# Performance work log

Measured on AMD Instinct MI355X. Metric: run time of the kernel, lower is better.

The kernel has to match this reference:

```python
import jax, jax.numpy as jnp
import numpy as np

B, S, E, H, L = 16, 1024, 512, 8, 4
D = E // H  # head_dim = 64


def setup_inputs() -> dict:
    key = jax.random.key(0)
    ks = jax.random.split(key, 16)
    std = 0.02
    inp = {
        "q": jax.random.normal(ks[0], (B, S, E), jnp.float32),
        "k": jax.random.normal(ks[1], (B, S, E), jnp.float32),
        "v": jax.random.normal(ks[2], (B, S, E), jnp.float32),
        # standard Linear params (torch convention: W is (out, in))
        "Wq": jax.random.normal(ks[3], (E, E), jnp.float32) * std,
        "bq": jnp.zeros((E,), jnp.float32),
        "Wk": jax.random.normal(ks[4], (E, E), jnp.float32) * std,
        "bk": jnp.zeros((E,), jnp.float32),
        # WFLinear: shared weight elementwise-multiplied by per-language factor
        "Wv_share": jax.random.normal(ks[5], (E, E), jnp.float32) * std,
        "Wv_spec": 1.0 + jax.random.normal(ks[6], (L, E, E), jnp.float32) * std,
        "bv_share": jnp.zeros((E,), jnp.float32),
        "bv_spec": jax.random.normal(ks[7], (L, E), jnp.float32) * std,
        "Wo_share": jax.random.normal(ks[8], (E, E), jnp.float32) * std,
        "Wo_spec": 1.0 + jax.random.normal(ks[9], (L, E, E), jnp.float32) * std,
        "bo_share": jnp.zeros((E,), jnp.float32),
        "bo_spec": jax.random.normal(ks[10], (L, E), jnp.float32) * std,
        "mask": jax.random.randint(ks[11], (B, S), 0, 2, jnp.int32),
        "languageID": 1,
    }
    return inp


def reference(q, k, v, Wq, bq, Wk, bk, Wv_share, Wv_spec, bv_share, bv_spec,
              Wo_share, Wo_spec, bo_share, bo_spec, mask, languageID):
    scaling = D ** (-0.5)
    # projections (torch Linear: x @ W.T + b)
    Q = (q @ Wq.T + bq).reshape(B, S, H, D).transpose(0, 2, 1, 3) * scaling
    K = (k @ Wk.T + bk).reshape(B, S, H, D).transpose(0, 2, 1, 3)
    Wv = Wv_share * Wv_spec[languageID]
    bv = bv_share + bv_spec[languageID]
    V = (v @ Wv.T + bv).reshape(B, S, H, D).transpose(0, 2, 1, 3)
    # NOTE: faithful to original — Q already scaled by d_k^-0.5, and
    # AttentionWF divides by sqrt(d_k) AGAIN (effective scale 1/d_k).
    alpha = jnp.einsum("bhqd,bhkd->bhqk", Q, K) / np.float32(np.sqrt(D))
    m = (mask == 0)[:, None, None, :]  # (B,1,1,S) over key axis
    alpha = jnp.where(m, jnp.float32(-1e9), alpha)
    alpha = jax.nn.softmax(alpha, axis=-1)
    # dropout p=0.0 -> identity
    ctx = jnp.einsum("bhqk,bhkd->bhqd", alpha, V)  # (B,H,S,D)
    concat = ctx.transpose(0, 2, 1, 3).reshape(B, S, E)
    Wo = Wo_share * Wo_spec[languageID]
    bo = bo_share + bo_spec[languageID]
    return concat @ Wo.T + bo
```

## Files before the change

kernel.cpp:

```cpp
#include <hip/hip_runtime.h>

#define B_ 16
#define S_ 1024
#define E_ 512
#define H_ 8
#define D_ 64
#define L_ 4
#define M_ (B_*S_)

typedef unsigned short u16;
typedef __attribute__((ext_vector_type(8))) short bf16x8;
typedef __attribute__((ext_vector_type(4))) float f32x4;
typedef __attribute__((ext_vector_type(4))) unsigned uint4v;

__device__ __forceinline__ u16 f2bf(float x) {
  unsigned u = __float_as_uint(x);
  unsigned r = (u + 0x7fffu + ((u >> 16) & 1u)) >> 16;
  return (u16)r;
}
__device__ __forceinline__ ushort4 f2bf4(float4 f) {
  ushort4 u;
  u.x = f2bf(f.x); u.y = f2bf(f.y); u.z = f2bf(f.z); u.w = f2bf(f.w);
  return u;
}
__device__ __forceinline__ unsigned pk_bf16(float lo, float hi) {
  unsigned ul = __float_as_uint(lo) + 0x8000u;
  unsigned uh = __float_as_uint(hi) + 0x8000u;
#if __has_builtin(__builtin_amdgcn_perm)
  return __builtin_amdgcn_perm(uh, ul, 0x07060302u);
#else
  return (ul >> 16) | (uh & 0xffff0000u);
#endif
}

typedef __attribute__((address_space(1))) const void gconst_void;
typedef __attribute__((address_space(3))) void lds_void;
__device__ __forceinline__ void gl_lds16(const void* g, void* l) {
  __builtin_amdgcn_global_load_lds((gconst_void*)g, (lds_void*)l, 16, 0, 0);
}

__global__ __launch_bounds__(256) void prep_w(
    const float* __restrict__ Wq, const float* __restrict__ Wk,
    const float* __restrict__ Wv_sh, const float* __restrict__ Wv_sp,
    const float* __restrict__ Wo_sh, const float* __restrict__ Wo_sp,
    const float* __restrict__ bv_sh, const float* __restrict__ bv_sp,
    const float* __restrict__ bo_sh, const float* __restrict__ bo_sp,
    const int* __restrict__ langp,
    u16* __restrict__ Wq_b, u16* __restrict__ Wk_b,
    u16* __restrict__ Wv_b, u16* __restrict__ Wo_b,
    float* __restrict__ bv_f, float* __restrict__ bo_f) {
  int lang = langp[0];
  int i = blockIdx.x * 256 + threadIdx.x;
  size_t wofs = (size_t)lang * (E_*E_/4) + i;
  ((ushort4*)Wq_b)[i] = f2bf4(((const float4*)Wq)[i]);
  ((ushort4*)Wk_b)[i] = f2bf4(((const float4*)Wk)[i]);
  float4 vs = ((const float4*)Wv_sh)[i], vp = ((const float4*)Wv_sp)[wofs];
  float4 os = ((const float4*)Wo_sh)[i], op = ((const float4*)Wo_sp)[wofs];
  float4 vv = {vs.x*vp.x, vs.y*vp.y, vs.z*vp.z, vs.w*vp.w};
  float4 oo = {os.x*op.x, os.y*op.y, os.z*op.z, os.w*op.w};
  ((ushort4*)Wv_b)[i] = f2bf4(vv);
  ((ushort4*)Wo_b)[i] = f2bf4(oo);
  if (i < E_/4) {
    float4 b1 = ((const float4*)bv_sh)[i], b2 = ((const float4*)(bv_sp + (size_t)lang*E_))[i];
    float4 b3 = ((const float4*)bo_sh)[i], b4 = ((const float4*)(bo_sp + (size_t)lang*E_))[i];
    float4 r1 = {b1.x+b2.x, b1.y+b2.y, b1.z+b2.z, b1.w+b2.w};
    float4 r2 = {b3.x+b4.x, b3.y+b4.y, b3.z+b4.z, b3.w+b4.w};
    ((float4*)bv_f)[i] = r1;
    ((float4*)bo_f)[i] = r2;
  }
}

__global__ __launch_bounds__(256) void gemm_qkv(
    const float* __restrict__ q, const float* __restrict__ k, const float* __restrict__ v,
    const u16* __restrict__ Wq_b, const u16* __restrict__ Wk_b, const u16* __restrict__ Wv_b,
    const float* __restrict__ bq, const float* __restrict__ bk, const float* __restrict__ bv,
    u16* __restrict__ Qb, u16* __restrict__ Kb, u16* __restrict__ Vb) {
  __shared__ __align__(16) float sAf[128*32];
  __shared__ __align__(16) u16 sB[128*32];
  const int z = blockIdx.z;
  const float* A    = (z == 0) ? q : (z == 1) ? k : v;
  const u16*   Bw   = (z == 0) ? Wq_b : (z == 1) ? Wk_b : Wv_b;
  const float* bias = (z == 0) ? bq : (z == 1) ? bk : bv;
  u16*         out  = (z == 0) ? Qb : (z == 1) ? Kb : Vb;
  const int t = threadIdx.x;
  const int m0 = blockIdx.y * 128, n0 = blockIdx.x * 128;
  const int lane = t & 63, wid = t >> 6;
  const int m16 = lane & 15, qq = lane >> 4;
  const int wrow = (wid >> 1) * 64, wcol = (wid & 1) * 64;
  f32x4 acc[4][4] = {};
  const int ca0 = wid*4;
  const float* ap[4];
  float* sap[4];
#pragma unroll
  for (int i = 0; i < 4; ++i) {
    int ca = ca0 + i;
    ap[i]  = A + (size_t)(m0 + ca*8 + (lane >> 3)) * E_ + (lane & 7) * 4;
    sap[i] = &sAf[ca * 256];
  }
  const int cb0 = wid*2, cb1 = wid*2 + 1;
  const u16* bp0 = Bw + (size_t)(n0 + cb0*16 + (lane >> 2)) * E_ + (lane & 3) * 8;
  const u16* bp1 = Bw + (size_t)(n0 + cb1*16 + (lane >> 2)) * E_ + (lane & 3) * 8;
  u16* sbp0 = &sB[cb0 * 512];
  u16* sbp1 = &sB[cb1 * 512];
  for (int k0 = 0; k0 < E_; k0 += 32) {
#pragma unroll
    for (int i = 0; i < 4; ++i) gl_lds16(ap[i], sap[i]);
    gl_lds16(bp0, sbp0);
    gl_lds16(bp1, sbp1);
    __syncthreads();
    bf16x8 af[4], bfm[4];
#pragma unroll
    for (int mt = 0; mt < 4; ++mt) {
      const float* ar = &sAf[(wrow + mt*16 + m16) * 32 + qq*8];
      f32x4 a0 = *(const f32x4*)ar;
      f32x4 a1 = *(const f32x4*)(ar + 4);
      union { uint4v u; bf16x8 h; } cv;
      cv.u = (uint4v){ pk_bf16(a0[0], a0[1]), pk_bf16(a0[2], a0[3]),
                       pk_bf16(a1[0], a1[1]), pk_bf16(a1[2], a1[3]) };
      af[mt] = cv.h;
    }
#pragma unroll
    for (int nt = 0; nt < 4; ++nt)
      bfm[nt] = *(const bf16x8*)&sB[(wcol + nt*16 + m16) * 32 + qq*8];
#pragma unroll
    for (int mt = 0; mt < 4; ++mt)
#pragma unroll
      for (int nt = 0; nt < 4; ++nt)
        acc[mt][nt] = __builtin_amdgcn_mfma_f32_16x16x32_bf16(af[mt], bfm[nt], acc[mt][nt], 0, 0, 0);
    __syncthreads();
#pragma unroll
    for (int i = 0; i < 4; ++i) ap[i] += 32;
    bp0 += 32; bp1 += 32;
  }
  float bvv[4];
#pragma unroll
  for (int nt = 0; nt < 4; ++nt) bvv[nt] = bias[n0 + wcol + nt*16 + m16];
#pragma unroll
  for (int mt = 0; mt < 4; ++mt) {
    int gm = m0 + wrow + mt*16 + qq*4;
#pragma unroll
    for (int nt = 0; nt < 4; ++nt) {
      int gn = n0 + wcol + nt*16 + m16;
#pragma unroll
      for (int r = 0; r < 4; ++r)
        out[(size_t)(gm + r) * E_ + gn] = f2bf(acc[mt][nt][r] + bvv[nt]);
    }
  }
}

__global__ __launch_bounds__(256) void gemm_lds(
    const u16* __restrict__ A, const u16* __restrict__ Bw,
    const float* __restrict__ bias, float* __restrict__ out) {
  __shared__ __align__(16) u16 sA[128*32];
  __shared__ __align__(16) u16 sB[128*32];
  const int t = threadIdx.x;
  const int m0 = blockIdx.y * 128, n0 = blockIdx.x * 128;
  const int lane = t & 63, wid = t >> 6;
  const int m16 = lane & 15, qq = lane >> 4;
  const int wrow = (wid >> 1) * 64, wcol = (wid & 1) * 64;
  f32x4 acc[4][4] = {};
  const int c0 = 2*wid, c1 = 2*wid + 1;
  const int colk = (lane & 3) * 8;
  const int r0 = c0*16 + (lane >> 2), r1 = c1*16 + (lane >> 2);
  const u16* a0 = A  + (size_t)(m0 + r0) * E_ + colk;
  const u16* a1 = A  + (size_t)(m0 + r1) * E_ + colk;
  const u16* b0 = Bw + (size_t)(n0 + r0) * E_ + colk;
  const u16* b1 = Bw + (size_t)(n0 + r1) * E_ + colk;
  u16* sa0 = &sA[c0*512]; u16* sa1 = &sA[c1*512];
  u16* sb0 = &sB[c0*512]; u16* sb1 = &sB[c1*512];
  for (int k0 = 0; k0 < E_; k0 += 32) {
    gl_lds16(a0, sa0);
    gl_lds16(a1, sa1);
    gl_lds16(b0, sb0);
    gl_lds16(b1, sb1);
    __syncthreads();
    bf16x8 af[4], bfm[4];
#pragma unroll
    for (int mt = 0; mt < 4; ++mt)
      af[mt] = *(const bf16x8*)&sA[(wrow + mt*16 + m16) * 32 + qq*8];
#pragma unroll
    for (int nt = 0; nt < 4; ++nt)
      bfm[nt] = *(const bf16x8*)&sB[(wcol + nt*16 + m16) * 32 + qq*8];
#pragma unroll
    for (int mt = 0; mt < 4; ++mt)
#pragma unroll
      for (int nt = 0; nt < 4; ++nt)
        acc[mt][nt] = __builtin_amdgcn_mfma_f32_16x16x32_bf16(af[mt], bfm[nt], acc[mt][nt], 0, 0, 0);
    __syncthreads();
    a0 += 32; a1 += 32; b0 += 32; b1 += 32;
  }
  float bv[4];
#pragma unroll
  for (int nt = 0; nt < 4; ++nt) bv[nt] = bias[n0 + wcol + nt*16 + m16];
#pragma unroll
  for (int mt = 0; mt < 4; ++mt) {
    int gm = m0 + wrow + mt*16 + qq*4;
#pragma unroll
    for (int nt = 0; nt < 4; ++nt) {
      int gn = n0 + wcol + nt*16 + m16;
#pragma unroll
      for (int r = 0; r < 4; ++r)
        out[(size_t)(gm + r) * E_ + gn] = acc[mt][nt][r] + bv[nt];
    }
  }
}

#define TS_ 72
__global__ __launch_bounds__(256) void transpose_v(const u16* __restrict__ Vb,
                                                   u16* __restrict__ Vt) {
  __shared__ __align__(16) u16 sT[64*TS_];
  const int t = threadIdx.x;
  const int bh = blockIdx.y, b = bh >> 3, h = bh & 7;
  const int s0 = blockIdx.x * 64;
  const int row = t >> 2, c0 = (t & 3) * 16;
  const u16* src = Vb + (size_t)(b*S_ + s0 + row) * E_ + h*D_ + c0;
  *(uint4*)&sT[row*TS_ + c0]     = *(const uint4*)src;
  *(uint4*)&sT[row*TS_ + c0 + 8] = *(const uint4*)(src + 8);
  __syncthreads();
  const int d = t >> 2, sc = (t & 3) * 16;
  unsigned w[8];
#pragma unroll
  for (int i = 0; i < 8; ++i) {
    unsigned lo = sT[(sc + 2*i    ) * TS_ + d];
    unsigned hi = sT[(sc + 2*i + 1) * TS_ + d];
    w[i] = lo | (hi << 16);
  }
  u16* dst = Vt + ((size_t)(b*H_ + h) * D_ + d) * S_ + s0 + sc;
  uint4 p0 = {w[0], w[1], w[2], w[3]}, p1 = {w[4], w[5], w[6], w[7]};
  *(uint4*)dst = p0;
  *(uint4*)(dst + 8) = p1;
}

#define KST 72
__global__ __launch_bounds__(256) void attn_mfma(
    const u16* __restrict__ Qb, const u16* __restrict__ Kb, const u16* __restrict__ Vt,
    const int* __restrict__ mask, u16* __restrict__ ctxb) {
  __shared__ __align__(16) u16 sK[64*KST];
  __shared__ __align__(16) u16 sV[64*KST];
  __shared__ __align__(16) u16 sP[64*KST];
  __shared__ __align__(16) float sMask[64];
  __shared__ __align__(16) float sL[64];
  const int t = threadIdx.x;
  const int lane = t & 63, w = t >> 6;
  const int m16 = lane & 15, quad = lane >> 4;
  const int bh = blockIdx.y, b = bh >> 3, h = bh & 7;
  const int qblk = blockIdx.x * 64;
  const int q0 = qblk + w * 16;
  bf16x8 qf0, qf1;
  {
    const u16* qp = Qb + (size_t)(b*S_ + q0 + m16) * E_ + h*D_ + quad*8;
    qf0 = *(const bf16x8*)qp;
    qf1 = *(const bf16x8*)(qp + 32);
  }
  f32x4 oacc[4] = {};
  float lpart = 0.f;
  const int srow = t >> 2, sc0 = (t & 3) * 16;
  const u16* kp = Kb + (size_t)(b*S_ + srow) * E_ + h*D_ + sc0;
  const u16* vp = Vt + ((size_t)(b*H_ + h) * D_ + srow) * S_ + sc0;
  uint4 rk0 = *(const uint4*)kp, rk1 = *(const uint4*)(kp + 8);
  uint4 rv0 = *(const uint4*)vp, rv1 = *(const uint4*)(vp + 8);
  float rmsk = 0.f;
  if (t < 64) rmsk = (mask[b*S_ + t] == 0) ? -1e9f : 0.f;
  const float CS = 0.015625f * 1.44269504f;
  for (int kt = 0; kt < S_; kt += 64) {
    *(uint4*)&sK[srow*KST + sc0]     = rk0;
    *(uint4*)&sK[srow*KST + sc0 + 8] = rk1;
    *(uint4*)&sV[srow*KST + sc0]     = rv0;
    *(uint4*)&sV[srow*KST + sc0 + 8] = rv1;
    if (t < 64) sMask[t] = rmsk;
    __syncthreads();
    if (kt + 64 < S_) {
      kp += (size_t)64 * E_; vp += 64;
      rk0 = *(const uint4*)kp; rk1 = *(const uint4*)(kp + 8);
      rv0 = *(const uint4*)vp; rv1 = *(const uint4*)(vp + 8);
      if (t < 64) rmsk = (mask[b*S_ + kt + 64 + t] == 0) ? -1e9f : 0.f;
    }
    f32x4 sacc[4] = {};
#pragma unroll
    for (int ct = 0; ct < 4; ++ct) {
      bf16x8 kf0 = *(const bf16x8*)&sK[(ct*16 + m16)*KST + quad*8];
      bf16x8 kf1 = *(const bf16x8*)&sK[(ct*16 + m16)*KST + 32 + quad*8];
      sacc[ct] = __builtin_amdgcn_mfma_f32_16x16x32_bf16(kf0, qf0, sacc[ct], 0, 0, 0);
      sacc[ct] = __builtin_amdgcn_mfma_f32_16x16x32_bf16(kf1, qf1, sacc[ct], 0, 0, 0);
    }
#pragma unroll
    for (int ct = 0; ct < 4; ++ct) {
      f32x4 msk = *(const f32x4*)&sMask[ct*16 + quad*4];
      float p0 = exp2f(fmaf(sacc[ct][0], CS, msk[0]));
      float p1 = exp2f(fmaf(sacc[ct][1], CS, msk[1]));
      float p2 = exp2f(fmaf(sacc[ct][2], CS, msk[2]));
      float p3 = exp2f(fmaf(sacc[ct][3], CS, msk[3]));
      lpart += (p0 + p1) + (p2 + p3);
      uint2 pq = { pk_bf16(p0, p1), pk_bf16(p2, p3) };
      *(uint2*)&sP[(w*16 + m16)*KST + ct*16 + quad*4] = pq;
    }
    bf16x8 pf0 = *(const bf16x8*)&sP[(w*16 + m16)*KST + quad*8];
    bf16x8 pf1 = *(const bf16x8*)&sP[(w*16 + m16)*KST + 32 + quad*8];
#pragma unroll
    for (int dt = 0; dt < 4; ++dt) {
      bf16x8 vf0 = *(const bf16x8*)&sV[(dt*16 + m16)*KST + quad*8];
      bf16x8 vf1 = *(const bf16x8*)&sV[(dt*16 + m16)*KST + 32 + quad*8];
      oacc[dt] = __builtin_amdgcn_mfma_f32_16x16x32_bf16(pf0, vf0, oacc[dt], 0, 0, 0);
      oacc[dt] = __builtin_amdgcn_mfma_f32_16x16x32_bf16(pf1, vf1, oacc[dt], 0, 0, 0);
    }
    __syncthreads();
  }
  lpart += __shfl_xor(lpart, 16);
  lpart += __shfl_xor(lpart, 32);
  if (quad == 0) sL[w*16 + m16] = lpart;
  float inv[4];
#pragma unroll
  for (int r = 0; r < 4; ++r) inv[r] = 1.0f / sL[w*16 + quad*4 + r];
#pragma unroll
  for (int dt = 0; dt < 4; ++dt)
#pragma unroll
    for (int r = 0; r < 4; ++r)
      sP[(w*16 + quad*4 + r)*KST + dt*16 + m16] = f2bf(oacc[dt][r] * inv[r]);
  __syncthreads();
  const int orow = t >> 2, oc0 = (t & 3) * 16;
  uint4 o0 = *(uint4*)&sP[orow*KST + oc0];
  uint4 o1 = *(uint4*)&sP[orow*KST + oc0 + 8];
  u16* dst = ctxb + (size_t)(b*S_ + qblk + orow) * E_ + h*D_ + oc0;
  *(uint4*)dst = o0;
  *(uint4*)(dst + 8) = o1;
}

extern "C" void kernel_launch(void* const* d_in, const int* in_sizes, int n_in,
                              void* d_out, int out_size, void* d_ws, size_t ws_size,
                              hipStream_t stream) {
  const float* q     = (const float*)d_in[0];
  const float* k     = (const float*)d_in[1];
  const float* v     = (const float*)d_in[2];
  const float* Wq    = (const float*)d_in[3];
  const float* bq    = (const float*)d_in[4];
  const float* Wk    = (const float*)d_in[5];
  const float* bk    = (const float*)d_in[6];
  const float* Wv_sh = (const float*)d_in[7];
  const float* Wv_sp = (const float*)d_in[8];
  const float* bv_sh = (const float*)d_in[9];
  const float* bv_sp = (const float*)d_in[10];
  const float* Wo_sh = (const float*)d_in[11];
  const float* Wo_sp = (const float*)d_in[12];
  const float* bo_sh = (const float*)d_in[13];
  const float* bo_sp = (const float*)d_in[14];
  const int*   mask  = (const int*)d_in[15];
  const int*   lang  = (const int*)d_in[16];

  char* ws = (char*)d_ws;
  size_t off = 0;
  auto alloc = [&](size_t bytes) -> char* {
    char* p = ws + off;
    off += (bytes + 255) & ~(size_t)255;
    return p;
  };
  u16* Qb   = (u16*)alloc((size_t)M_ * E_ * 2);
  u16* Kb   = (u16*)alloc((size_t)M_ * E_ * 2);
  u16* Vb   = (u16*)alloc((size_t)M_ * E_ * 2);
  u16* Vt   = (u16*)alloc((size_t)M_ * E_ * 2);
  u16* ctxb = (u16*)alloc((size_t)M_ * E_ * 2);
  u16* Wq_b = (u16*)alloc((size_t)E_ * E_ * 2);
  u16* Wk_b = (u16*)alloc((size_t)E_ * E_ * 2);
  u16* Wv_b = (u16*)alloc((size_t)E_ * E_ * 2);
  u16* Wo_b = (u16*)alloc((size_t)E_ * E_ * 2);
  float* bv_f = (float*)alloc(E_ * 4);
  float* bo_f = (float*)alloc(E_ * 4);

  prep_w<<<E_*E_/1024, 256, 0, stream>>>(Wq, Wk, Wv_sh, Wv_sp, Wo_sh, Wo_sp,
                                         bv_sh, bv_sp, bo_sh, bo_sp, lang,
                                         Wq_b, Wk_b, Wv_b, Wo_b, bv_f, bo_f);

  dim3 qkvgrid(E_/128, M_/128, 3);
  gemm_qkv<<<qkvgrid, 256, 0, stream>>>(q, k, v, Wq_b, Wk_b, Wv_b,
                                        bq, bk, bv_f, Qb, Kb, Vb);

  dim3 tgrid(S_/64, B_*H_);
  transpose_v<<<tgrid, 256, 0, stream>>>(Vb, Vt);

  dim3 agrid(S_/64, B_*H_);
  attn_mfma<<<agrid, 256, 0, stream>>>(Qb, Kb, Vt, mask, ctxb);

  dim3 ggrid(E_/128, M_/128);
  gemm_lds<<<ggrid, 256, 0, stream>>>(ctxb, Wo_b, bo_f, (float*)d_out);
}
```

Measured before the change: 316.9 us.

## Fuse V transpose into QKV GEMM, double K-step GEMMs, widen attention query tile

```diff
diff --git a/kernel.cpp b/kernel.cpp
--- a/kernel.cpp
+++ b/kernel.cpp
@@ -74,76 +74,110 @@
     const float* __restrict__ q, const float* __restrict__ k, const float* __restrict__ v,
     const u16* __restrict__ Wq_b, const u16* __restrict__ Wk_b, const u16* __restrict__ Wv_b,
     const float* __restrict__ bq, const float* __restrict__ bk, const float* __restrict__ bv,
-    u16* __restrict__ Qb, u16* __restrict__ Kb, u16* __restrict__ Vb) {
-  __shared__ __align__(16) float sAf[128*32];
-  __shared__ __align__(16) u16 sB[128*32];
+    u16* __restrict__ Qb, u16* __restrict__ Kb, u16* __restrict__ Vt) {
+  __shared__ __align__(16) float sAf[2*128*32];
+  __shared__ __align__(16) u16 sB[2*128*32];
   const int z = blockIdx.z;
   const float* A    = (z == 0) ? q : (z == 1) ? k : v;
   const u16*   Bw   = (z == 0) ? Wq_b : (z == 1) ? Wk_b : Wv_b;
   const float* bias = (z == 0) ? bq : (z == 1) ? bk : bv;
-  u16*         out  = (z == 0) ? Qb : (z == 1) ? Kb : Vb;
   const int t = threadIdx.x;
   const int m0 = blockIdx.y * 128, n0 = blockIdx.x * 128;
   const int lane = t & 63, wid = t >> 6;
   const int m16 = lane & 15, qq = lane >> 4;
   const int wrow = (wid >> 1) * 64, wcol = (wid & 1) * 64;
   f32x4 acc[4][4] = {};
-  const int ca0 = wid*4;
-  const float* ap[4];
-  float* sap[4];
-#pragma unroll
-  for (int i = 0; i < 4; ++i) {
-    int ca = ca0 + i;
-    ap[i]  = A + (size_t)(m0 + ca*8 + (lane >> 3)) * E_ + (lane & 7) * 4;
-    sap[i] = &sAf[ca * 256];
-  }
-  const int cb0 = wid*2, cb1 = wid*2 + 1;
-  const u16* bp0 = Bw + (size_t)(n0 + cb0*16 + (lane >> 2)) * E_ + (lane & 3) * 8;
-  const u16* bp1 = Bw + (size_t)(n0 + cb1*16 + (lane >> 2)) * E_ + (lane & 3) * 8;
-  u16* sbp0 = &sB[cb0 * 512];
-  u16* sbp1 = &sB[cb1 * 512];
-  for (int k0 = 0; k0 < E_; k0 += 32) {
-#pragma unroll
-    for (int i = 0; i < 4; ++i) gl_lds16(ap[i], sap[i]);
-    gl_lds16(bp0, sbp0);
-    gl_lds16(bp1, sbp1);
-    __syncthreads();
-    bf16x8 af[4], bfm[4];
+  const float* apg[2][4];
+  float* apl[2][4];
+#pragma unroll
+  for (int p = 0; p < 2; ++p)
+#pragma unroll
+    for (int i = 0; i < 4; ++i) {
+      int ca = wid*4 + i;
+      apg[p][i] = A + (size_t)(m0 + ca*8 + (lane >> 3)) * E_ + p*32 + (lane & 7) * 4;
+      apl[p][i] = &sAf[p*4096 + ca*256 + lane*4];
+    }
+  const u16* bpg[2][2];
+  u16* bpl[2][2];
+#pragma unroll
+  for (int p = 0; p < 2; ++p)
+#pragma unroll
+    for (int i = 0; i < 2; ++i) {
+      int cb = wid*2 + i;
+      bpg[p][i] = Bw + (size_t)(n0 + cb*16 + (lane >> 2)) * E_ + p*32 + (lane & 3) * 8;
+      bpl[p][i] = &sB[p*4096 + cb*512 + lane*8];
+    }
+  for (int k0 = 0; k0 < E_; k0 += 64) {
+#pragma unroll
+    for (int p = 0; p < 2; ++p) {
+#pragma unroll
+      for (int i = 0; i < 4; ++i) gl_lds16(apg[p][i], apl[p][i]);
+#pragma unroll
+      for (int i = 0; i < 2; ++i) gl_lds16(bpg[p][i], bpl[p][i]);
+    }
+    __syncthreads();
+#pragma unroll
+    for (int p = 0; p < 2; ++p) {
+      bf16x8 af[4], bfm[4];
+#pragma unroll
+      for (int mt = 0; mt < 4; ++mt) {
+        const float* ar = &sAf[p*4096 + (wrow + mt*16 + m16) * 32 + qq*8];
+        f32x4 a0 = *(const f32x4*)ar;
+        f32x4 a1 = *(const f32x4*)(ar + 4);
+        union { uint4v u; bf16x8 h; } cv;
+        cv.u = (uint4v){ pk_bf16(a0[0], a0[1]), pk_bf16(a0[2], a0[3]),
+                         pk_bf16(a1[0], a1[1]), pk_bf16(a1[2], a1[3]) };
+        af[mt] = cv.h;
+      }
+#pragma unroll
+      for (int nt = 0; nt < 4; ++nt)
+        bfm[nt] = *(const bf16x8*)&sB[p*4096 + (wcol + nt*16 + m16) * 32 + qq*8];
+#pragma unroll
+      for (int mt = 0; mt < 4; ++mt)
+#pragma unroll
+        for (int nt = 0; nt < 4; ++nt)
+          acc[mt][nt] = __builtin_amdgcn_mfma_f32_16x16x32_bf16(af[mt], bfm[nt], acc[mt][nt], 0, 0, 0);
+    }
+    __syncthreads();
+#pragma unroll
+    for (int p = 0; p < 2; ++p) {
+#pragma unroll
+      for (int i = 0; i < 4; ++i) apg[p][i] += 64;
+#pragma unroll
+      for (int i = 0; i < 2; ++i) bpg[p][i] += 64;
+    }
+  }
+  float bvv[4];
+#pragma unroll
+  for (int nt = 0; nt < 4; ++nt) bvv[nt] = bias[n0 + wcol + nt*16 + m16];
+  if (z < 2) {
+    u16* out = (z == 0) ? Qb : Kb;
 #pragma unroll
     for (int mt = 0; mt < 4; ++mt) {
-      const float* ar = &sAf[(wrow + mt*16 + m16) * 32 + qq*8];
-      f32x4 a0 = *(const f32x4*)ar;
-      f32x4 a1 = *(const f32x4*)(ar + 4);
-      union { uint4v u; bf16x8 h; } cv;
-      cv.u = (uint4v){ pk_bf16(a0[0], a0[1]), pk_bf16(a0[2], a0[3]),
-                       pk_bf16(a1[0], a1[1]), pk_bf16(a1[2], a1[3]) };
-      af[mt] = cv.h;
-    }
-#pragma unroll
-    for (int nt = 0; nt < 4; ++nt)
-      bfm[nt] = *(const bf16x8*)&sB[(wcol + nt*16 + m16) * 32 + qq*8];
-#pragma unroll
-    for (int mt = 0; mt < 4; ++mt)
-#pragma unroll
-      for (int nt = 0; nt < 4; ++nt)
-        acc[mt][nt] = __builtin_amdgcn_mfma_f32_16x16x32_bf16(af[mt], bfm[nt], acc[mt][nt], 0, 0, 0);
-    __syncthreads();
-#pragma unroll
-    for (int i = 0; i < 4; ++i) ap[i] += 32;
-    bp0 += 32; bp1 += 32;
-  }
-  float bvv[4];
-#pragma unroll
-  for (int nt = 0; nt < 4; ++nt) bvv[nt] = bias[n0 + wcol + nt*16 + m16];
-#pragma unroll
-  for (int mt = 0; mt < 4; ++mt) {
-    int gm = m0 + wrow + mt*16 + qq*4;
-#pragma unroll
-    for (int nt = 0; nt < 4; ++nt) {
-      int gn = n0 + wcol + nt*16 + m16;
-#pragma unroll
-      for (int r = 0; r < 4; ++r)
-        out[(size_t)(gm + r) * E_ + gn] = f2bf(acc[mt][nt][r] + bvv[nt]);
+      int gm = m0 + wrow + mt*16 + qq*4;
+#pragma unroll
+      for (int nt = 0; nt < 4; ++nt) {
+        int gn = n0 + wcol + nt*16 + m16;
+#pragma unroll
+        for (int r = 0; r < 4; ++r)
+          out[(size_t)(gm + r) * E_ + gn] = f2bf(acc[mt][nt][r] + bvv[nt]);
+      }
+    }
+  } else {
+#pragma unroll
+    for (int mt = 0; mt < 4; ++mt) {
+      int gm = m0 + wrow + mt*16 + qq*4;
+      int b = gm >> 10, s0 = gm & (S_ - 1);
+#pragma unroll
+      for (int nt = 0; nt < 4; ++nt) {
+        int gn = n0 + wcol + nt*16 + m16;
+        ushort4 u;
+        u.x = f2bf(acc[mt][nt][0] + bvv[nt]);
+        u.y = f2bf(acc[mt][nt][1] + bvv[nt]);
+        u.z = f2bf(acc[mt][nt][2] + bvv[nt]);
+        u.w = f2bf(acc[mt][nt][3] + bvv[nt]);
+        *(ushort4*)&Vt[((size_t)(b*E_ + gn)) * S_ + s0] = u;
+      }
     }
   }
 }
@@ -151,43 +185,55 @@
 __global__ __launch_bounds__(256) void gemm_lds(
     const u16* __restrict__ A, const u16* __restrict__ Bw,
     const float* __restrict__ bias, float* __restrict__ out) {
-  __shared__ __align__(16) u16 sA[128*32];
-  __shared__ __align__(16) u16 sB[128*32];
+  __shared__ __align__(16) u16 sA[2*128*32];
+  __shared__ __align__(16) u16 sB[2*128*32];
   const int t = threadIdx.x;
   const int m0 = blockIdx.y * 128, n0 = blockIdx.x * 128;
   const int lane = t & 63, wid = t >> 6;
   const int m16 = lane & 15, qq = lane >> 4;
   const int wrow = (wid >> 1) * 64, wcol = (wid & 1) * 64;
   f32x4 acc[4][4] = {};
-  const int c0 = 2*wid, c1 = 2*wid + 1;
-  const int colk = (lane & 3) * 8;
-  const int r0 = c0*16 + (lane >> 2), r1 = c1*16 + (lane >> 2);
-  const u16* a0 = A  + (size_t)(m0 + r0) * E_ + colk;
-  const u16* a1 = A  + (size_t)(m0 + r1) * E_ + colk;
-  const u16* b0 = Bw + (size_t)(n0 + r0) * E_ + colk;
-  const u16* b1 = Bw + (size_t)(n0 + r1) * E_ + colk;
-  u16* sa0 = &sA[c0*512]; u16* sa1 = &sA[c1*512];
-  u16* sb0 = &sB[c0*512]; u16* sb1 = &sB[c1*512];
-  for (int k0 = 0; k0 < E_; k0 += 32) {
-    gl_lds16(a0, sa0);
-    gl_lds16(a1, sa1);
-    gl_lds16(b0, sb0);
-    gl_lds16(b1, sb1);
-    __syncthreads();
-    bf16x8 af[4], bfm[4];
-#pragma unroll
-    for (int mt = 0; mt < 4; ++mt)
-      af[mt] = *(const bf16x8*)&sA[(wrow + mt*16 + m16) * 32 + qq*8];
-#pragma unroll
-    for (int nt = 0; nt < 4; ++nt)
-      bfm[nt] = *(const bf16x8*)&sB[(wcol + nt*16 + m16) * 32 + qq*8];
-#pragma unroll
-    for (int mt = 0; mt < 4; ++mt)
+  const u16* apg[2][2]; u16* apl[2][2];
+  const u16* bpg[2][2]; u16* bpl[2][2];
+#pragma unroll
+  for (int p = 0; p < 2; ++p)
+#pragma unroll
+    for (int i = 0; i < 2; ++i) {
+      int c = wid*2 + i;
+      apg[p][i] = A  + (size_t)(m0 + c*16 + (lane >> 2)) * E_ + p*32 + (lane & 3) * 8;
+      bpg[p][i] = Bw + (size_t)(n0 + c*16 + (lane >> 2)) * E_ + p*32 + (lane & 3) * 8;
+      apl[p][i] = &sA[p*4096 + c*512 + lane*8];
+      bpl[p][i] = &sB[p*4096 + c*512 + lane*8];
+    }
+  for (int k0 = 0; k0 < E_; k0 += 64) {
+#pragma unroll
+    for (int p = 0; p < 2; ++p)
+#pragma unroll
+      for (int i = 0; i < 2; ++i) {
+        gl_lds16(apg[p][i], apl[p][i]);
+        gl_lds16(bpg[p][i], bpl[p][i]);
+      }
+    __syncthreads();
+#pragma unroll
+    for (int p = 0; p < 2; ++p) {
+      bf16x8 af[4], bfm[4];
+#pragma unroll
+      for (int mt = 0; mt < 4; ++mt)
+        af[mt] = *(const bf16x8*)&sA[p*4096 + (wrow + mt*16 + m16) * 32 + qq*8];
 #pragma unroll
       for (int nt = 0; nt < 4; ++nt)
-        acc[mt][nt] = __builtin_amdgcn_mfma_f32_16x16x32_bf16(af[mt], bfm[nt], acc[mt][nt], 0, 0, 0);
-    __syncthreads();
-    a0 += 32; a1 += 32; b0 += 32; b1 += 32;
+        bfm[nt] = *(const bf16x8*)&sB[p*4096 + (wcol + nt*16 + m16) * 32 + qq*8];
+#pragma unroll
+      for (int mt = 0; mt < 4; ++mt)
+#pragma unroll
+        for (int nt = 0; nt < 4; ++nt)
+          acc[mt][nt] = __builtin_amdgcn_mfma_f32_16x16x32_bf16(af[mt], bfm[nt], acc[mt][nt], 0, 0, 0);
+    }
+    __syncthreads();
+#pragma unroll
+    for (int p = 0; p < 2; ++p)
+#pragma unroll
+      for (int i = 0; i < 2; ++i) { apg[p][i] += 64; bpg[p][i] += 64; }
   }
   float bv[4];
 #pragma unroll
@@ -203,32 +249,6 @@
         out[(size_t)(gm + r) * E_ + gn] = acc[mt][nt][r] + bv[nt];
     }
   }
-}
-
-#define TS_ 72
-__global__ __launch_bounds__(256) void transpose_v(const u16* __restrict__ Vb,
-                                                   u16* __restrict__ Vt) {
-  __shared__ __align__(16) u16 sT[64*TS_];
-  const int t = threadIdx.x;
-  const int bh = blockIdx.y, b = bh >> 3, h = bh & 7;
-  const int s0 = blockIdx.x * 64;
-  const int row = t >> 2, c0 = (t & 3) * 16;
-  const u16* src = Vb + (size_t)(b*S_ + s0 + row) * E_ + h*D_ + c0;
-  *(uint4*)&sT[row*TS_ + c0]     = *(const uint4*)src;
-  *(uint4*)&sT[row*TS_ + c0 + 8] = *(const uint4*)(src + 8);
-  __syncthreads();
-  const int d = t >> 2, sc = (t & 3) * 16;
-  unsigned w[8];
-#pragma unroll
-  for (int i = 0; i < 8; ++i) {
-    unsigned lo = sT[(sc + 2*i    ) * TS_ + d];
-    unsigned hi = sT[(sc + 2*i + 1) * TS_ + d];
-    w[i] = lo | (hi << 16);
-  }
-  u16* dst = Vt + ((size_t)(b*H_ + h) * D_ + d) * S_ + s0 + sc;
-  uint4 p0 = {w[0], w[1], w[2], w[3]}, p1 = {w[4], w[5], w[6], w[7]};
-  *(uint4*)dst = p0;
-  *(uint4*)(dst + 8) = p1;
 }
 
 #define KST 72
@@ -237,26 +257,27 @@
     const int* __restrict__ mask, u16* __restrict__ ctxb) {
   __shared__ __align__(16) u16 sK[64*KST];
   __shared__ __align__(16) u16 sV[64*KST];
-  __shared__ __align__(16) u16 sP[64*KST];
+  __shared__ __align__(16) u16 sP[128*KST];
   __shared__ __align__(16) float sMask[64];
-  __shared__ __align__(16) float sL[64];
+  __shared__ __align__(16) float sL[128];
   const int t = threadIdx.x;
   const int lane = t & 63, w = t >> 6;
   const int m16 = lane & 15, quad = lane >> 4;
   const int bh = blockIdx.y, b = bh >> 3, h = bh & 7;
-  const int qblk = blockIdx.x * 64;
-  const int q0 = qblk + w * 16;
-  bf16x8 qf0, qf1;
-  {
-    const u16* qp = Qb + (size_t)(b*S_ + q0 + m16) * E_ + h*D_ + quad*8;
-    qf0 = *(const bf16x8*)qp;
-    qf1 = *(const bf16x8*)(qp + 32);
-  }
-  f32x4 oacc[4] = {};
-  float lpart = 0.f;
+  const int qblk = blockIdx.x * 128;
+  const int q0 = qblk + w * 32;
+  bf16x8 qf[2][2];
+#pragma unroll
+  for (int f = 0; f < 2; ++f) {
+    const u16* qp = Qb + (size_t)(b*S_ + q0 + f*16 + m16) * E_ + h*D_ + quad*8;
+    qf[f][0] = *(const bf16x8*)qp;
+    qf[f][1] = *(const bf16x8*)(qp + 32);
+  }
+  f32x4 oacc[2][4] = {};
+  float lpart[2] = {0.f, 0.f};
   const int srow = t >> 2, sc0 = (t & 3) * 16;
   const u16* kp = Kb + (size_t)(b*S_ + srow) * E_ + h*D_ + sc0;
-  const u16* vp = Vt + ((size_t)(b*H_ + h) * D_ + srow) * S_ + sc0;
+  const u16* vp = Vt + ((size_t)(b*E_ + h*D_) + srow) * S_ + sc0;
   uint4 rk0 = *(const uint4*)kp, rk1 = *(const uint4*)(kp + 8);
   uint4 rv0 = *(const uint4*)vp, rv1 = *(const uint4*)(vp + 8);
   float rmsk = 0.f;
@@ -275,54 +296,76 @@
       rv0 = *(const uint4*)vp; rv1 = *(const uint4*)(vp + 8);
       if (t < 64) rmsk = (mask[b*S_ + kt + 64 + t] == 0) ? -1e9f : 0.f;
     }
-    f32x4 sacc[4] = {};
+    f32x4 sacc[2][4] = {};
 #pragma unroll
     for (int ct = 0; ct < 4; ++ct) {
       bf16x8 kf0 = *(const bf16x8*)&sK[(ct*16 + m16)*KST + quad*8];
       bf16x8 kf1 = *(const bf16x8*)&sK[(ct*16 + m16)*KST + 32 + quad*8];
-      sacc[ct] = __builtin_amdgcn_mfma_f32_16x16x32_bf16(kf0, qf0, sacc[ct], 0, 0, 0);
-      sacc[ct] = __builtin_amdgcn_mfma_f32_16x16x32_bf16(kf1, qf1, sacc[ct], 0, 0, 0);
-    }
-#pragma unroll
-    for (int ct = 0; ct < 4; ++ct) {
-      f32x4 msk = *(const f32x4*)&sMask[ct*16 + quad*4];
-      float p0 = exp2f(fmaf(sacc[ct][0], CS, msk[0]));
-      float p1 = exp2f(fmaf(sacc[ct][1], CS, msk[1]));
-      float p2 = exp2f(fmaf(sacc[ct][2], CS, msk[2]));
-      float p3 = exp2f(fmaf(sacc[ct][3], CS, msk[3]));
-      lpart += (p0 + p1) + (p2 + p3);
-      uint2 pq = { pk_bf16(p0, p1), pk_bf16(p2, p3) };
-      *(uint2*)&sP[(w*16 + m16)*KST + ct*16 + quad*4] = pq;
-    }
-    bf16x8 pf0 = *(const bf16x8*)&sP[(w*16 + m16)*KST + quad*8];
-    bf16x8 pf1 = *(const bf16x8*)&sP[(w*16 + m16)*KST + 32 + quad*8];
+      sacc[0][ct] = __builtin_amdgcn_mfma_f32_16x16x32_bf16(kf0, qf[0][0], sacc[0][ct], 0, 0, 0);
+      sacc[0][ct] = __builtin_amdgcn_mfma_f32_16x16x32_bf16(kf1, qf[0][1], sacc[0][ct], 0, 0, 0);
+      sacc[1][ct] = __builtin_amdgcn_mfma_f32_16x16x32_bf16(kf0, qf[1][0], sacc[1][ct], 0, 0, 0);
+      sacc[1][ct] = __builtin_amdgcn_mfma_f32_16x16x32_bf16(kf1, qf[1][1], sacc[1][ct], 0, 0, 0);
+    }
+#pragma unroll
+    for (int f = 0; f < 2; ++f) {
+#pragma unroll
+      for (int ct = 0; ct < 4; ++ct) {
+        f32x4 msk = *(const f32x4*)&sMask[ct*16 + quad*4];
+        float p0 = exp2f(fmaf(sacc[f][ct][0], CS, msk[0]));
+        float p1 = exp2f(fmaf(sacc[f][ct][1], CS, msk[1]));
+        float p2 = exp2f(fmaf(sacc[f][ct][2], CS, msk[2]));
+        float p3 = exp2f(fmaf(sacc[f][ct][3], CS, msk[3]));
+        lpart[f] += (p0 + p1) + (p2 + p3);
+        uint2 pq = { pk_bf16(p0, p1), pk_bf16(p2, p3) };
+        *(uint2*)&sP[(w*32 + f*16 + m16)*KST + ct*16 + quad*4] = pq;
+      }
+    }
+    bf16x8 pf[2][2];
+#pragma unroll
+    for (int f = 0; f < 2; ++f) {
+      pf[f][0] = *(const bf16x8*)&sP[(w*32 + f*16 + m16)*KST + quad*8];
+      pf[f][1] = *(const bf16x8*)&sP[(w*32 + f*16 + m16)*KST + 32 + quad*8];
+    }
 #pragma unroll
     for (int dt = 0; dt < 4; ++dt) {
       bf16x8 vf0 = *(const bf16x8*)&sV[(dt*16 + m16)*KST + quad*8];
       bf16x8 vf1 = *(const bf16x8*)&sV[(dt*16 + m16)*KST + 32 + quad*8];
-      oacc[dt] = __builtin_amdgcn_mfma_f32_16x16x32_bf16(pf0, vf0, oacc[dt], 0, 0, 0);
-      oacc[dt] = __builtin_amdgcn_mfma_f32_16x16x32_bf16(pf1, vf1, oacc[dt], 0, 0, 0);
-    }
-    __syncthreads();
-  }
-  lpart += __shfl_xor(lpart, 16);
-  lpart += __shfl_xor(lpart, 32);
-  if (quad == 0) sL[w*16 + m16] = lpart;
-  float inv[4];
-#pragma unroll
-  for (int r = 0; r < 4; ++r) inv[r] = 1.0f / sL[w*16 + quad*4 + r];
-#pragma unroll
-  for (int dt = 0; dt < 4; ++dt)
-#pragma unroll
-    for (int r = 0; r < 4; ++r)
-      sP[(w*16 + quad*4 + r)*KST + dt*16 + m16] = f2bf(oacc[dt][r] * inv[r]);
+      oacc[0][dt] = __builtin_amdgcn_mfma_f32_16x16x32_bf16(pf[0][0], vf0, oacc[0][dt], 0, 0, 0);
+      oacc[0][dt] = __builtin_amdgcn_mfma_f32_16x16x32_bf16(pf[0][1], vf1, oacc[0][dt], 0, 0, 0);
+      oacc[1][dt] = __builtin_amdgcn_mfma_f32_16x16x32_bf16(pf[1][0], vf0, oacc[1][dt], 0, 0, 0);
+      oacc[1][dt] = __builtin_amdgcn_mfma_f32_16x16x32_bf16(pf[1][1], vf1, oacc[1][dt], 0, 0, 0);
+    }
+    __syncthreads();
+  }
+#pragma unroll
+  for (int f = 0; f < 2; ++f) {
+    float l = lpart[f];
+    l += __shfl_xor(l, 16);
+    l += __shfl_xor(l, 32);
+    if (quad == 0) sL[w*32 + f*16 + m16] = l;
+  }
+#pragma unroll
+  for (int f = 0; f < 2; ++f) {
+    float inv[4];
+#pragma unroll
+    for (int r = 0; r < 4; ++r) inv[r] = 1.0f / sL[w*32 + f*16 + quad*4 + r];
+#pragma unroll
+    for (int dt = 0; dt < 4; ++dt)
+#pragma unroll
+      for (int r = 0; r < 4; ++r)
+        sP[(w*32 + f*16 + quad*4 + r)*KST + dt*16 + m16] = f2bf(oacc[f][dt][r] * inv[r]);
+  }
   __syncthreads();
-  const int orow = t >> 2, oc0 = (t & 3) * 16;
+  const int orow = t >> 1, oc0 = (t & 1) * 32;
   uint4 o0 = *(uint4*)&sP[orow*KST + oc0];
   uint4 o1 = *(uint4*)&sP[orow*KST + oc0 + 8];
+  uint4 o2 = *(uint4*)&sP[orow*KST + oc0 + 16];
+  uint4 o3 = *(uint4*)&sP[orow*KST + oc0 + 24];
   u16* dst = ctxb + (size_t)(b*S_ + qblk + orow) * E_ + h*D_ + oc0;
   *(uint4*)dst = o0;
   *(uint4*)(dst + 8) = o1;
+  *(uint4*)(dst + 16) = o2;
+  *(uint4*)(dst + 24) = o3;
 }
 
 extern "C" void kernel_launch(void* const* d_in, const int* in_sizes, int n_in,
@@ -355,7 +398,6 @@
   };
   u16* Qb   = (u16*)alloc((size_t)M_ * E_ * 2);
   u16* Kb   = (u16*)alloc((size_t)M_ * E_ * 2);
-  u16* Vb   = (u16*)alloc((size_t)M_ * E_ * 2);
   u16* Vt   = (u16*)alloc((size_t)M_ * E_ * 2);
   u16* ctxb = (u16*)alloc((size_t)M_ * E_ * 2);
   u16* Wq_b = (u16*)alloc((size_t)E_ * E_ * 2);
@@ -371,12 +413,9 @@
 
   dim3 qkvgrid(E_/128, M_/128, 3);
   gemm_qkv<<<qkvgrid, 256, 0, stream>>>(q, k, v, Wq_b, Wk_b, Wv_b,
-                                        bq, bk, bv_f, Qb, Kb, Vb);
-
-  dim3 tgrid(S_/64, B_*H_);
-  transpose_v<<<tgrid, 256, 0, stream>>>(Vb, Vt);
-
-  dim3 agrid(S_/64, B_*H_);
+                                        bq, bk, bv_f, Qb, Kb, Vt);
+
+  dim3 agrid(S_/128, B_*H_);
   attn_mfma<<<agrid, 256, 0, stream>>>(Qb, Kb, Vt, mask, ctxb);
 
   dim3 ggrid(E_/128, M_/128);
```

Measured after the change: 321.9 us. About the same (+1.6%).
